# Performance work log

Hardware: AMD Instinct MI355X
Metric: run time of the kernel (lower is better)

Reference implementation:

```python
import jax, jax.numpy as jnp
import numpy as np

N = 65536          # nodes
E = 1_048_576      # edges (avg degree 16)
IN_DIM = 16        # input_irreps = 16x0e
OUT_DIM = 8        # output_irreps = 8x0e
S_MUL = 32         # hidden 0e multiplicity
V_MUL = 16         # hidden 1o multiplicity
HID = S_MUL + 3 * V_MUL  # 80
LAYERS = 3
DEG = 16.0


def fctp(feat, eattr, w1, w2, w3, w4):
    """FullyConnectedTensorProduct(hidden x '1x0e+1x1o' -> hidden) per edge.
    Paths: 0e*0e->0e, 1o*1o->0e (dot, CG 1/sqrt(3)), 0e*1o->1o, 1o*0e->1o.
    Path weights mix multiplicities; e3nn-style fan-in normalization."""
    s1 = feat[:, :S_MUL]                         # [E, 32]
    v1 = feat[:, S_MUL:].reshape(-1, V_MUL, 3)   # [E, 16, 3]
    s2 = eattr[:, 0]                             # [E]
    v2 = eattr[:, 1:4]                           # [E, 3]
    c = 1.0 / np.sqrt(2.0)  # two paths per output irrep
    out_s = c * (jnp.einsum('ea,e,ac->ec', s1, s2, w1) / np.sqrt(S_MUL)
                 + jnp.einsum('eak,ek,ac->ec', v1, v2, w2) / np.sqrt(3.0 * V_MUL))
    out_v = c * (jnp.einsum('ea,ek,ac->eck', s1, v2, w3) / np.sqrt(S_MUL)
                 + jnp.einsum('eak,e,ac->eck', v1, s2, w4) / np.sqrt(V_MUL))
    return jnp.concatenate([out_s, out_v.reshape(-1, 3 * V_MUL)], axis=-1)


def setup_inputs() -> dict:
    key = jax.random.key(0)
    ks = jax.random.split(key, 12)
    inp = {
        'x': jax.random.normal(ks[0], (N, IN_DIM), jnp.float32),
        'edge_index': jax.random.randint(ks[1], (2, E), 0, N, jnp.int64 if jax.config.jax_enable_x64 else jnp.int32),
        'edge_attr': jax.random.normal(ks[2], (E, 4), jnp.float32),
        'W_in': jax.random.normal(ks[3], (IN_DIM, HID), jnp.float32) / np.sqrt(IN_DIM),
        'b_in': jnp.zeros((HID,), jnp.float32),
        'tp_w1': jax.random.normal(ks[4], (LAYERS, S_MUL, S_MUL), jnp.float32),
        'tp_w2': jax.random.normal(ks[5], (LAYERS, V_MUL, S_MUL), jnp.float32),
        'tp_w3': jax.random.normal(ks[6], (LAYERS, S_MUL, V_MUL), jnp.float32),
        'tp_w4': jax.random.normal(ks[7], (LAYERS, V_MUL, V_MUL), jnp.float32),
        'W_out': jax.random.normal(ks[8], (HID, OUT_DIM), jnp.float32) / np.sqrt(HID),
        'b_out': jnp.zeros((OUT_DIM,), jnp.float32),
    }
    return inp


def reference(x, edge_index, edge_attr, W_in, b_in, tp_w1, tp_w2, tp_w3, tp_w4, W_out, b_out):
    src, dst = edge_index[0], edge_index[1]
    h = x @ W_in + b_in                                   # [N, 80]
    for l in range(LAYERS):
        m = fctp(h[src], edge_attr, tp_w1[l], tp_w2[l], tp_w3[l], tp_w4[l])  # [E, 80]
        h = jax.ops.segment_sum(m, dst, num_segments=N) / np.sqrt(DEG)       # [N, 80]
    h = jax.nn.relu(h)
    return h @ W_out + b_out                              # [N, 8]
```

## Files before the change

kernel.cpp:

```cpp
#include <hip/hip_runtime.h>

#define NN 65536
#define NE 1048576
#define HID 80
#define TCAP 8192
#define ECAP 8192
#define LCAP 4864

typedef unsigned int u32;
typedef unsigned short u16;
typedef unsigned long long u64;

typedef float v4f __attribute__((ext_vector_type(4)));

__device__ __forceinline__ u16 f2bf(float f) {
  u32 u = __float_as_uint(f);
  u = (u + 0x7fffu + ((u >> 16) & 1u)) >> 16;
  return (u16)u;
}
__device__ __forceinline__ float bfhi(u32 packed) {
  return __uint_as_float(packed & 0xffff0000u);
}
__device__ __forceinline__ float bflo(u32 packed) {
  return __uint_as_float(packed << 16);
}
__device__ __forceinline__ float4 ntload4f(const float4* p) {
  v4f v = __builtin_nontemporal_load((const v4f*)p);
  return make_float4(v.x, v.y, v.z, v.w);
}
__device__ __forceinline__ int ntloadi(const int* p) {
  return __builtin_nontemporal_load(p);
}

__global__ __launch_bounds__(256) void k_p1_in(const int* __restrict__ dst,
    const int* __restrict__ src, const float4* __restrict__ eattr,
    int* __restrict__ bcnt, uint4* __restrict__ tmp,
    const float* __restrict__ x, const float* __restrict__ W,
    const float* __restrict__ b, u16* __restrict__ hmain,
    u16* __restrict__ htail) {
  if (blockIdx.x < 512) {
    __shared__ int hist[256];
    __shared__ int lofs[257];
    __shared__ int gbase[256];
    __shared__ int sc[256];
    __shared__ uint4 buf[2048];
    __shared__ unsigned char bkid[2048];
    int t = threadIdx.x;
    hist[t] = 0;
    __syncthreads();
    uint4 rec[8];
    int bk[8], lr[8];
    int base = blockIdx.x * 2048 + t;
#pragma unroll
    for (int k = 0; k < 8; k++) {
      int idx = base + k * 256;
      int d = ntloadi(dst + idx);
      float4 ea = ntload4f(eattr + idx);
      int s = ntloadi(src + idx);
      u32 c01 = (u32)f2bf(ea.x) | ((u32)f2bf(ea.y) << 16);
      u32 c23 = (u32)f2bf(ea.z) | ((u32)f2bf(ea.w) << 16);
      rec[k] = make_uint4((u32)s, c01, c23, (u32)d);
      bk[k] = d >> 8;
      lr[k] = atomicAdd(&hist[bk[k]], 1);
    }
    __syncthreads();
    int h = hist[t];
    gbase[t] = atomicAdd(&bcnt[t], h);
    sc[t] = h;
    __syncthreads();
    for (int d = 1; d < 256; d <<= 1) {
      int v = (t >= d) ? sc[t - d] : 0;
      __syncthreads();
      sc[t] += v;
      __syncthreads();
    }
    lofs[t] = sc[t] - h;
    if (t == 255) lofs[256] = 2048;
    __syncthreads();
#pragma unroll
    for (int k = 0; k < 8; k++) {
      int slot = lofs[bk[k]] + lr[k];
      buf[slot] = rec[k];
      bkid[slot] = (unsigned char)bk[k];
    }
    __syncthreads();
#pragma unroll
    for (int k = 0; k < 8; k++) {
      int j = t + k * 256;
      int lo = bkid[j];
      tmp[(size_t)lo * TCAP + gbase[lo] + (j - lofs[lo])] = buf[j];
    }
  } else {
    int idx = (blockIdx.x - 512) * 256 + threadIdx.x;
    if (idx >= NN * 10) return;
    int n = idx / 10, part = idx % 10;
    const float4* xr = (const float4*)(x + (size_t)n * 16);
    float4 x0 = xr[0], x1 = xr[1], x2 = xr[2], x3 = xr[3];
    const float xs[16] = {x0.x, x0.y, x0.z, x0.w, x1.x, x1.y, x1.z, x1.w,
                          x2.x, x2.y, x2.z, x2.w, x3.x, x3.y, x3.z, x3.w};
    float acc[8];
#pragma unroll
    for (int j = 0; j < 8; j++) acc[j] = b[part * 8 + j];
#pragma unroll
    for (int k = 0; k < 16; k++) {
#pragma unroll
      for (int j = 0; j < 8; j++) acc[j] += xs[k] * W[k * HID + part * 8 + j];
    }
    u32 p0 = (u32)f2bf(acc[0]) | ((u32)f2bf(acc[1]) << 16);
    u32 p1 = (u32)f2bf(acc[2]) | ((u32)f2bf(acc[3]) << 16);
    u32 p2 = (u32)f2bf(acc[4]) | ((u32)f2bf(acc[5]) << 16);
    u32 p3 = (u32)f2bf(acc[6]) | ((u32)f2bf(acc[7]) << 16);
    uint4 vv = make_uint4(p0, p1, p2, p3);
    if (part < 8)
      *(uint4*)(hmain + (size_t)n * 64 + part * 8) = vv;
    else
      *(uint4*)(htail + (size_t)n * 16 + (part - 8) * 8) = vv;
  }
}

__global__ __launch_bounds__(512) void k_p2m(const int* __restrict__ bcnt,
    const uint4* __restrict__ tmp, int* __restrict__ counts_tot,
    int* __restrict__ offs_fin, uint4* __restrict__ erec,
    int* __restrict__ brank, int* __restrict__ bidx, int* __restrict__ dcnt) {
  extern __shared__ uint4 rbuf[];
  __shared__ int hist[256];
  __shared__ int sc[256];
  __shared__ int noff[256];
  __shared__ int cur[256];
  int t = threadIdx.x;
  if (t < 256) {
    hist[t] = 0;
    cur[t] = 0;
  }
  __syncthreads();
  int b = blockIdx.x;
  int cnt = min(bcnt[b], LCAP);
  const uint4* tb = tmp + (size_t)b * TCAP;
  for (int j = t; j < cnt; j += 512) {
    uint4 r = tb[j];
    rbuf[j] = r;
    atomicAdd(&hist[r.w & 255], 1);
  }
  __syncthreads();
  int deg = 0;
  if (t < 256) {
    deg = hist[t];
    sc[t] = (deg + 7) & ~7;
  }
  __syncthreads();
  for (int d = 1; d < 256; d <<= 1) {
    int v = (t < 256 && t >= d) ? sc[t - d] : 0;
    __syncthreads();
    if (t < 256) sc[t] += v;
    __syncthreads();
  }
  if (t < 256) {
    int p = (deg + 7) & ~7;
    int off = b * ECAP + sc[t] - p;
    noff[t] = off;
    offs_fin[b * 256 + t] = off;
    counts_tot[b * 256 + t] = deg;
  }
  __syncthreads();
  for (int j = t; j < cnt; j += 512) {
    uint4 r = rbuf[j];
    int i = r.w & 255;
    int lr = atomicAdd(&cur[i], 1);
    erec[(size_t)noff[i] + lr] = make_uint4(r.x, r.y, r.z, 0u);
  }
  __syncthreads();
  if (t < 256) {
    int degp = (deg + 7) & ~7;
    uint4 z = make_uint4(0u, 0u, 0u, 0u);
    for (int e = deg; e < degp; e++) erec[(size_t)noff[t] + e] = z;
    int n = b * 256 + t;
    int bb2 = 15 - min(degp >> 3, 15);
    int lane = t & 63;
    int base = 0;
#pragma unroll 1
    for (int bb = 0; bb < 16; bb++) {
      u64 m = __ballot(bb2 == bb);
      if (bb2 == bb) {
        int leader = __ffsll((long long)m) - 1;
        int lr = __popcll(m & ((lane == 63) ? ~0ull >> 1 : ((1ull << lane) - 1)));
        int bs = 0;
        if (lane == leader) bs = atomicAdd(&dcnt[bb], __popcll(m));
        bs = __shfl(bs, leader, 64);
        base = bs + lr;
      }
    }
    brank[n] = base;
    bidx[n] = bb2;
  }
}

__global__ __launch_bounds__(256) void k_p3(const int* __restrict__ dcnt,
    const int* __restrict__ brank, const int* __restrict__ bidx,
    int* __restrict__ nperm) {
  __shared__ int dsum[16];
  int t = threadIdx.x;
  if (t < 16) {
    int v = dcnt[t];
    int incl = v;
#pragma unroll
    for (int d = 1; d < 16; d <<= 1) {
      int o = __shfl_up(incl, d, 64);
      if (t >= d) incl += o;
    }
    dsum[t] = incl - v;
  }
  __syncthreads();
  int n = blockIdx.x * 256 + t;
  nperm[dsum[bidx[n]] + brank[n]] = n;
}

template <int LAST>
__global__ __launch_bounds__(128, 3) void k_msg(const u16* __restrict__ hmain,
    const u16* __restrict__ htail, u16* __restrict__ omain,
    u16* __restrict__ otail,
    const float* __restrict__ w1, const float* __restrict__ w2,
    const float* __restrict__ w3, const float* __restrict__ w4,
    const int* __restrict__ offsets, const int* __restrict__ counts,
    const int* __restrict__ nperm, const uint4* __restrict__ erec,
    const float* __restrict__ Wout, const float* __restrict__ bout,
    float* __restrict__ outp) {
  __shared__ float Rlds[8][4][81];
  int tid = threadIdx.x;
  const int q = tid >> 4;
  const int c = tid & 15;
  const int n = nperm[blockIdx.x * 8 + q];

  float R[4][5];
#pragma unroll
  for (int j = 0; j < 4; j++)
#pragma unroll
    for (int i = 0; i < 5; i++) R[j][i] = 0.f;

  const int start = offsets[n];
  const int degp = (counts[n] + 7) & ~7;
  const int B = degp >> 3;
  const uint2* hrow = (const uint2*)hmain + c;
  const u16* trow = htail + c;

  int i = 0;
  for (; i + 2 <= B; i += 2) {
    const int baseA = start + 8 * i;
    const int baseB = baseA + 8;
    uint4 rA[8], rB[8];
#pragma unroll
    for (int k = 0; k < 8; k++) rA[k] = erec[baseA + k];
#pragma unroll
    for (int k = 0; k < 8; k++) rB[k] = erec[baseB + k];
    uint2 hA[8], hB[8];
    u32 tA[8], tB[8];
#pragma unroll
    for (int k = 0; k < 8; k++) {
      size_t s16 = (size_t)rA[k].x * 16;
      hA[k] = hrow[s16];
      tA[k] = trow[s16];
    }
#pragma unroll
    for (int k = 0; k < 8; k++) {
      size_t s16 = (size_t)rB[k].x * 16;
      hB[k] = hrow[s16];
      tB[k] = trow[s16];
    }
#pragma unroll
    for (int k = 0; k < 8; k++) {
      float A0 = bflo(hA[k].x), A1 = bfhi(hA[k].x);
      float A2 = bflo(hA[k].y), A3 = bfhi(hA[k].y);
      float A4 = bflo(tA[k]);
      float f0 = bflo(rA[k].y), f1 = bfhi(rA[k].y);
      float f2 = bflo(rA[k].z), f3 = bfhi(rA[k].z);
      R[0][0] += f0 * A0; R[0][1] += f0 * A1; R[0][2] += f0 * A2;
      R[0][3] += f0 * A3; R[0][4] += f0 * A4;
      R[1][0] += f1 * A0; R[1][1] += f1 * A1; R[1][2] += f1 * A2;
      R[1][3] += f1 * A3; R[1][4] += f1 * A4;
      R[2][0] += f2 * A0; R[2][1] += f2 * A1; R[2][2] += f2 * A2;
      R[2][3] += f2 * A3; R[2][4] += f2 * A4;
      R[3][0] += f3 * A0; R[3][1] += f3 * A1; R[3][2] += f3 * A2;
      R[3][3] += f3 * A3; R[3][4] += f3 * A4;
    }
#pragma unroll
    for (int k = 0; k < 8; k++) {
      float A0 = bflo(hB[k].x), A1 = bfhi(hB[k].x);
      float A2 = bflo(hB[k].y), A3 = bfhi(hB[k].y);
      float A4 = bflo(tB[k]);
      float f0 = bflo(rB[k].y), f1 = bfhi(rB[k].y);
      float f2 = bflo(rB[k].z), f3 = bfhi(rB[k].z);
      R[0][0] += f0 * A0; R[0][1] += f0 * A1; R[0][2] += f0 * A2;
      R[0][3] += f0 * A3; R[0][4] += f0 * A4;
      R[1][0] += f1 * A0; R[1][1] += f1 * A1; R[1][2] += f1 * A2;
      R[1][3] += f1 * A3; R[1][4] += f1 * A4;
      R[2][0] += f2 * A0; R[2][1] += f2 * A1; R[2][2] += f2 * A2;
      R[2][3] += f2 * A3; R[2][4] += f2 * A4;
      R[3][0] += f3 * A0; R[3][1] += f3 * A1; R[3][2] += f3 * A2;
      R[3][3] += f3 * A3; R[3][4] += f3 * A4;
    }
  }
  if (i < B) {
    const int baseA = start + 8 * i;
    uint4 rA[8];
#pragma unroll
    for (int k = 0; k < 8; k++) rA[k] = erec[baseA + k];
    uint2 hA[8];
    u32 tA[8];
#pragma unroll
    for (int k = 0; k < 8; k++) {
      size_t s16 = (size_t)rA[k].x * 16;
      hA[k] = hrow[s16];
      tA[k] = trow[s16];
    }
#pragma unroll
    for (int k = 0; k < 8; k++) {
      float A0 = bflo(hA[k].x), A1 = bfhi(hA[k].x);
      float A2 = bflo(hA[k].y), A3 = bfhi(hA[k].y);
      float A4 = bflo(tA[k]);
      float f0 = bflo(rA[k].y), f1 = bfhi(rA[k].y);
      float f2 = bflo(rA[k].z), f3 = bfhi(rA[k].z);
      R[0][0] += f0 * A0; R[0][1] += f0 * A1; R[0][2] += f0 * A2;
      R[0][3] += f0 * A3; R[0][4] += f0 * A4;
      R[1][0] += f1 * A0; R[1][1] += f1 * A1; R[1][2] += f1 * A2;
      R[1][3] += f1 * A3; R[1][4] += f1 * A4;
      R[2][0] += f2 * A0; R[2][1] += f2 * A1; R[2][2] += f2 * A2;
      R[2][3] += f2 * A3; R[2][4] += f2 * A4;
      R[3][0] += f3 * A0; R[3][1] += f3 * A1; R[3][2] += f3 * A2;
      R[3][3] += f3 * A3; R[3][4] += f3 * A4;
    }
  }

#pragma unroll
  for (int j = 0; j < 4; j++) {
#pragma unroll
    for (int k = 0; k < 4; k++) Rlds[q][j][4 * c + k] = R[j][k];
    Rlds[q][j][64 + c] = R[j][4];
  }

  const float C1 = 0.03125f;
  const float C2 = 0.025515518f;
  const float C3 = 0.03125f;
  const float C4 = 0.044194174f;

  u16* opm = omain + (size_t)n * 64;

  float s0 = 0.f, s1 = 0.f;
#pragma unroll
  for (int a = 0; a < 32; a++) {
    float rs = Rlds[q][0][a];
    s0 += rs * w1[a * 32 + c];
    s1 += rs * w1[a * 32 + c + 16];
  }
  float t0 = 0.f, t1 = 0.f;
#pragma unroll
  for (int a = 0; a < 16; a++) {
    float T = Rlds[q][1][32 + 3 * a] + Rlds[q][2][33 + 3 * a] +
              Rlds[q][3][34 + 3 * a];
    t0 += T * w2[a * 32 + c];
    t1 += T * w2[a * 32 + c + 16];
  }

  float y[8];
  if (LAST) {
#pragma unroll
    for (int j = 0; j < 8; j++) y[j] = 0.f;
    float vs0 = C1 * s0 + C2 * t0;
    float vs1 = C1 * s1 + C2 * t1;
    vs0 = vs0 > 0.f ? vs0 : 0.f;
    vs1 = vs1 > 0.f ? vs1 : 0.f;
#pragma unroll
    for (int j = 0; j < 8; j++)
      y[j] += vs0 * Wout[c * 8 + j] + vs1 * Wout[(c + 16) * 8 + j];
  } else {
    opm[c] = f2bf(C1 * s0 + C2 * t0);
    opm[c + 16] = f2bf(C1 * s1 + C2 * t1);
  }

#pragma unroll
  for (int v2 = 0; v2 < 3; v2++) {
    int c2 = 32 + 16 * v2 + c;
    int cv = (c2 - 32) / 3, k = (c2 - 32) % 3;
    float a3 = 0.f, a4 = 0.f;
#pragma unroll
    for (int a = 0; a < 32; a++) a3 += Rlds[q][k + 1][a] * w3[a * 16 + cv];
#pragma unroll
    for (int a = 0; a < 16; a++)
      a4 += Rlds[q][0][32 + 3 * a + k] * w4[a * 16 + cv];
    float val = C3 * a3 + C4 * a4;
    if (LAST) {
      val = val > 0.f ? val : 0.f;
#pragma unroll
      for (int j = 0; j < 8; j++) y[j] += val * Wout[c2 * 8 + j];
    } else {
      u16 v = f2bf(val);
      if (v2 < 2) opm[32 + 16 * v2 + c] = v;
      else otail[(size_t)n * 16 + c] = v;
    }
  }

  if (LAST) {
#pragma unroll
    for (int m = 1; m <= 8; m <<= 1) {
#pragma unroll
      for (int j = 0; j < 8; j++) y[j] += __shfl_xor(y[j], m, 64);
    }
    float w = y[0];
#pragma unroll
    for (int j = 1; j < 8; j++)
      if (c == j) w = y[j];
    if (c < 8) outp[(size_t)n * 8 + c] = w + bout[c];
  }
}

extern "C" void kernel_launch(void* const* d_in, const int* in_sizes, int n_in,
                              void* d_out, int out_size, void* d_ws,
                              size_t ws_size, hipStream_t stream) {
  const float* x = (const float*)d_in[0];
  const int* ei = (const int*)d_in[1];
  const float* eattr = (const float*)d_in[2];
  const float* W_in = (const float*)d_in[3];
  const float* b_in = (const float*)d_in[4];
  const float* tp_w1 = (const float*)d_in[5];
  const float* tp_w2 = (const float*)d_in[6];
  const float* tp_w3 = (const float*)d_in[7];
  const float* tp_w4 = (const float*)d_in[8];
  const float* W_out = (const float*)d_in[9];
  const float* b_out = (const float*)d_in[10];
  float* out = (float*)d_out;

  char* ws = (char*)d_ws;
  size_t off = 0;
  auto alloc = [&](size_t bytes) {
    void* p = ws + off;
    off += (bytes + 255) & ~size_t(255);
    return p;
  };
  u16* hm_a = (u16*)alloc((size_t)NN * 64 * 2);
  u16* ht_a = (u16*)alloc((size_t)NN * 16 * 2);
  u16* hm_b = (u16*)alloc((size_t)NN * 64 * 2);
  u16* ht_b = (u16*)alloc((size_t)NN * 16 * 2);
  int* bcnt = (int*)alloc(256 * 4);
  int* dcnt = (int*)alloc(16 * 4);
  int* counts_tot = (int*)alloc((size_t)NN * 4);
  int* offs_fin = (int*)alloc((size_t)NN * 4);
  int* brank = (int*)alloc((size_t)NN * 4);
  int* bidx = (int*)alloc((size_t)NN * 4);
  int* nperm = (int*)alloc((size_t)NN * 4);
  uint4* tmp = (uint4*)alloc((size_t)256 * TCAP * 16);
  uint4* erec = (uint4*)alloc((size_t)256 * ECAP * 16);

  const int* src = ei;
  const int* dst = ei + NE;

  hipMemsetAsync(bcnt, 0, 1024 + 64, stream);
  k_p1_in<<<512 + (NN * 10 + 255) / 256, 256, 0, stream>>>(
      dst, src, (const float4*)eattr, bcnt, tmp, x, W_in, b_in, hm_a, ht_a);
  k_p2m<<<256, 512, LCAP * 16, stream>>>(bcnt, tmp, counts_tot, offs_fin,
                                         erec, brank, bidx, dcnt);
  k_p3<<<256, 256, 0, stream>>>(dcnt, brank, bidx, nperm);

  u16* hmi = hm_a;
  u16* hti = ht_a;
  u16* hmo = hm_b;
  u16* hto = ht_b;
  for (int l = 0; l < 2; l++) {
    k_msg<0><<<NN / 8, 128, 0, stream>>>(hmi, hti, hmo, hto, tp_w1 + l * 1024,
                                         tp_w2 + l * 512, tp_w3 + l * 512,
                                         tp_w4 + l * 256, offs_fin, counts_tot,
                                         nperm, erec, W_out, b_out, out);
    u16* t;
    t = hmi; hmi = hmo; hmo = t;
    t = hti; hti = hto; hto = t;
  }
  k_msg<1><<<NN / 8, 128, 0, stream>>>(hmi, hti, hmo, hto, tp_w1 + 2048,
                                       tp_w2 + 1024, tp_w3 + 1024, tp_w4 + 512,
                                       offs_fin, counts_tot, nperm, erec,
                                       W_out, b_out, out);
}
```

Baseline: 340.2 us.

## Fold input projection into first message layer by aggregating raw x

Drops the separate input-projection pass that wrote bf16 h. The first layer now gathers the 16-wide fp32 x rows directly, accumulates edge-weighted sums of x plus sums of edge attributes, and then applies W_in and b_in after aggregation. Because the input projection is linear, this gives the same result while gathering fewer bytes per edge and skipping one write and read of h. In exchange it reads fp32 x instead of bf16 h and adds a small per-node matmul in the first layer.

Result: no change. 336.8 us (-1.0%).

```diff
diff --git a/kernel.cpp b/kernel.cpp
--- a/kernel.cpp
+++ b/kernel.cpp
@@ -32,89 +32,59 @@
   return __builtin_nontemporal_load(p);
 }
 
-__global__ __launch_bounds__(256) void k_p1_in(const int* __restrict__ dst,
+__global__ __launch_bounds__(256) void k_p1(const int* __restrict__ dst,
     const int* __restrict__ src, const float4* __restrict__ eattr,
-    int* __restrict__ bcnt, uint4* __restrict__ tmp,
-    const float* __restrict__ x, const float* __restrict__ W,
-    const float* __restrict__ b, u16* __restrict__ hmain,
-    u16* __restrict__ htail) {
-  if (blockIdx.x < 512) {
-    __shared__ int hist[256];
-    __shared__ int lofs[257];
-    __shared__ int gbase[256];
-    __shared__ int sc[256];
-    __shared__ uint4 buf[2048];
-    __shared__ unsigned char bkid[2048];
-    int t = threadIdx.x;
-    hist[t] = 0;
+    int* __restrict__ bcnt, uint4* __restrict__ tmp) {
+  __shared__ int hist[256];
+  __shared__ int lofs[257];
+  __shared__ int gbase[256];
+  __shared__ int sc[256];
+  __shared__ uint4 buf[2048];
+  __shared__ unsigned char bkid[2048];
+  int t = threadIdx.x;
+  hist[t] = 0;
+  __syncthreads();
+  uint4 rec[8];
+  int bk[8], lr[8];
+  int base = blockIdx.x * 2048 + t;
+#pragma unroll
+  for (int k = 0; k < 8; k++) {
+    int idx = base + k * 256;
+    int d = ntloadi(dst + idx);
+    float4 ea = ntload4f(eattr + idx);
+    int s = ntloadi(src + idx);
+    u32 c01 = (u32)f2bf(ea.x) | ((u32)f2bf(ea.y) << 16);
+    u32 c23 = (u32)f2bf(ea.z) | ((u32)f2bf(ea.w) << 16);
+    rec[k] = make_uint4((u32)s, c01, c23, (u32)d);
+    bk[k] = d >> 8;
+    lr[k] = atomicAdd(&hist[bk[k]], 1);
+  }
+  __syncthreads();
+  int h = hist[t];
+  gbase[t] = atomicAdd(&bcnt[t], h);
+  sc[t] = h;
+  __syncthreads();
+  for (int d = 1; d < 256; d <<= 1) {
+    int v = (t >= d) ? sc[t - d] : 0;
     __syncthreads();
-    uint4 rec[8];
-    int bk[8], lr[8];
-    int base = blockIdx.x * 2048 + t;
-#pragma unroll
-    for (int k = 0; k < 8; k++) {
-      int idx = base + k * 256;
-      int d = ntloadi(dst + idx);
-      float4 ea = ntload4f(eattr + idx);
-      int s = ntloadi(src + idx);
-      u32 c01 = (u32)f2bf(ea.x) | ((u32)f2bf(ea.y) << 16);
-      u32 c23 = (u32)f2bf(ea.z) | ((u32)f2bf(ea.w) << 16);
-      rec[k] = make_uint4((u32)s, c01, c23, (u32)d);
-      bk[k] = d >> 8;
-      lr[k] = atomicAdd(&hist[bk[k]], 1);
-    }
+    sc[t] += v;
     __syncthreads();
-    int h = hist[t];
-    gbase[t] = atomicAdd(&bcnt[t], h);
-    sc[t] = h;
-    __syncthreads();
-    for (int d = 1; d < 256; d <<= 1) {
-      int v = (t >= d) ? sc[t - d] : 0;
-      __syncthreads();
-      sc[t] += v;
-      __syncthreads();
-    }
-    lofs[t] = sc[t] - h;
-    if (t == 255) lofs[256] = 2048;
-    __syncthreads();
-#pragma unroll
-    for (int k = 0; k < 8; k++) {
-      int slot = lofs[bk[k]] + lr[k];
-      buf[slot] = rec[k];
-      bkid[slot] = (unsigned char)bk[k];
-    }
-    __syncthreads();
-#pragma unroll
-    for (int k = 0; k < 8; k++) {
-      int j = t + k * 256;
-      int lo = bkid[j];
-      tmp[(size_t)lo * TCAP + gbase[lo] + (j - lofs[lo])] = buf[j];
-    }
-  } else {
-    int idx = (blockIdx.x - 512) * 256 + threadIdx.x;
-    if (idx >= NN * 10) return;
-    int n = idx / 10, part = idx % 10;
-    const float4* xr = (const float4*)(x + (size_t)n * 16);
-    float4 x0 = xr[0], x1 = xr[1], x2 = xr[2], x3 = xr[3];
-    const float xs[16] = {x0.x, x0.y, x0.z, x0.w, x1.x, x1.y, x1.z, x1.w,
-                          x2.x, x2.y, x2.z, x2.w, x3.x, x3.y, x3.z, x3.w};
-    float acc[8];
-#pragma unroll
-    for (int j = 0; j < 8; j++) acc[j] = b[part * 8 + j];
-#pragma unroll
-    for (int k = 0; k < 16; k++) {
-#pragma unroll
-      for (int j = 0; j < 8; j++) acc[j] += xs[k] * W[k * HID + part * 8 + j];
-    }
-    u32 p0 = (u32)f2bf(acc[0]) | ((u32)f2bf(acc[1]) << 16);
-    u32 p1 = (u32)f2bf(acc[2]) | ((u32)f2bf(acc[3]) << 16);
-    u32 p2 = (u32)f2bf(acc[4]) | ((u32)f2bf(acc[5]) << 16);
-    u32 p3 = (u32)f2bf(acc[6]) | ((u32)f2bf(acc[7]) << 16);
-    uint4 vv = make_uint4(p0, p1, p2, p3);
-    if (part < 8)
-      *(uint4*)(hmain + (size_t)n * 64 + part * 8) = vv;
-    else
-      *(uint4*)(htail + (size_t)n * 16 + (part - 8) * 8) = vv;
+  }
+  lofs[t] = sc[t] - h;
+  if (t == 255) lofs[256] = 2048;
+  __syncthreads();
+#pragma unroll
+  for (int k = 0; k < 8; k++) {
+    int slot = lofs[bk[k]] + lr[k];
+    buf[slot] = rec[k];
+    bkid[slot] = (unsigned char)bk[k];
+  }
+  __syncthreads();
+#pragma unroll
+  for (int k = 0; k < 8; k++) {
+    int j = t + k * 256;
+    int lo = bkid[j];
+    tmp[(size_t)lo * TCAP + gbase[lo] + (j - lofs[lo])] = buf[j];
   }
 }
 
@@ -214,7 +184,7 @@
   nperm[dsum[bidx[n]] + brank[n]] = n;
 }
 
-template <int LAST>
+template <int LAST, int FIRST>
 __global__ __launch_bounds__(128, 3) void k_msg(const u16* __restrict__ hmain,
     const u16* __restrict__ htail, u16* __restrict__ omain,
     u16* __restrict__ otail,
@@ -223,117 +193,201 @@
     const int* __restrict__ offsets, const int* __restrict__ counts,
     const int* __restrict__ nperm, const uint4* __restrict__ erec,
     const float* __restrict__ Wout, const float* __restrict__ bout,
-    float* __restrict__ outp) {
+    float* __restrict__ outp,
+    const float* __restrict__ xg, const float* __restrict__ Win,
+    const float* __restrict__ bin) {
   __shared__ float Rlds[8][4][81];
+  __shared__ float Mlds[8][4][16];
   int tid = threadIdx.x;
   const int q = tid >> 4;
   const int c = tid & 15;
   const int n = nperm[blockIdx.x * 8 + q];
 
-  float R[4][5];
-#pragma unroll
-  for (int j = 0; j < 4; j++)
-#pragma unroll
-    for (int i = 0; i < 5; i++) R[j][i] = 0.f;
-
   const int start = offsets[n];
   const int degp = (counts[n] + 7) & ~7;
   const int B = degp >> 3;
-  const uint2* hrow = (const uint2*)hmain + c;
-  const u16* trow = htail + c;
-
-  int i = 0;
-  for (; i + 2 <= B; i += 2) {
-    const int baseA = start + 8 * i;
-    const int baseB = baseA + 8;
-    uint4 rA[8], rB[8];
-#pragma unroll
-    for (int k = 0; k < 8; k++) rA[k] = erec[baseA + k];
-#pragma unroll
-    for (int k = 0; k < 8; k++) rB[k] = erec[baseB + k];
-    uint2 hA[8], hB[8];
-    u32 tA[8], tB[8];
-#pragma unroll
-    for (int k = 0; k < 8; k++) {
-      size_t s16 = (size_t)rA[k].x * 16;
-      hA[k] = hrow[s16];
-      tA[k] = trow[s16];
-    }
-#pragma unroll
-    for (int k = 0; k < 8; k++) {
-      size_t s16 = (size_t)rB[k].x * 16;
-      hB[k] = hrow[s16];
-      tB[k] = trow[s16];
-    }
-#pragma unroll
-    for (int k = 0; k < 8; k++) {
-      float A0 = bflo(hA[k].x), A1 = bfhi(hA[k].x);
-      float A2 = bflo(hA[k].y), A3 = bfhi(hA[k].y);
-      float A4 = bflo(tA[k]);
-      float f0 = bflo(rA[k].y), f1 = bfhi(rA[k].y);
-      float f2 = bflo(rA[k].z), f3 = bfhi(rA[k].z);
-      R[0][0] += f0 * A0; R[0][1] += f0 * A1; R[0][2] += f0 * A2;
-      R[0][3] += f0 * A3; R[0][4] += f0 * A4;
-      R[1][0] += f1 * A0; R[1][1] += f1 * A1; R[1][2] += f1 * A2;
-      R[1][3] += f1 * A3; R[1][4] += f1 * A4;
-      R[2][0] += f2 * A0; R[2][1] += f2 * A1; R[2][2] += f2 * A2;
-      R[2][3] += f2 * A3; R[2][4] += f2 * A4;
-      R[3][0] += f3 * A0; R[3][1] += f3 * A1; R[3][2] += f3 * A2;
-      R[3][3] += f3 * A3; R[3][4] += f3 * A4;
-    }
-#pragma unroll
-    for (int k = 0; k < 8; k++) {
-      float A0 = bflo(hB[k].x), A1 = bfhi(hB[k].x);
-      float A2 = bflo(hB[k].y), A3 = bfhi(hB[k].y);
-      float A4 = bflo(tB[k]);
-      float f0 = bflo(rB[k].y), f1 = bfhi(rB[k].y);
-      float f2 = bflo(rB[k].z), f3 = bfhi(rB[k].z);
-      R[0][0] += f0 * A0; R[0][1] += f0 * A1; R[0][2] += f0 * A2;
-      R[0][3] += f0 * A3; R[0][4] += f0 * A4;
-      R[1][0] += f1 * A0; R[1][1] += f1 * A1; R[1][2] += f1 * A2;
-      R[1][3] += f1 * A3; R[1][4] += f1 * A4;
-      R[2][0] += f2 * A0; R[2][1] += f2 * A1; R[2][2] += f2 * A2;
-      R[2][3] += f2 * A3; R[2][4] += f2 * A4;
-      R[3][0] += f3 * A0; R[3][1] += f3 * A1; R[3][2] += f3 * A2;
-      R[3][3] += f3 * A3; R[3][4] += f3 * A4;
-    }
-  }
-  if (i < B) {
-    const int baseA = start + 8 * i;
-    uint4 rA[8];
-#pragma unroll
-    for (int k = 0; k < 8; k++) rA[k] = erec[baseA + k];
-    uint2 hA[8];
-    u32 tA[8];
-#pragma unroll
-    for (int k = 0; k < 8; k++) {
-      size_t s16 = (size_t)rA[k].x * 16;
-      hA[k] = hrow[s16];
-      tA[k] = trow[s16];
-    }
-#pragma unroll
-    for (int k = 0; k < 8; k++) {
-      float A0 = bflo(hA[k].x), A1 = bfhi(hA[k].x);
-      float A2 = bflo(hA[k].y), A3 = bfhi(hA[k].y);
-      float A4 = bflo(tA[k]);
-      float f0 = bflo(rA[k].y), f1 = bfhi(rA[k].y);
-      float f2 = bflo(rA[k].z), f3 = bfhi(rA[k].z);
-      R[0][0] += f0 * A0; R[0][1] += f0 * A1; R[0][2] += f0 * A2;
-      R[0][3] += f0 * A3; R[0][4] += f0 * A4;
-      R[1][0] += f1 * A0; R[1][1] += f1 * A1; R[1][2] += f1 * A2;
-      R[1][3] += f1 * A3; R[1][4] += f1 * A4;
-      R[2][0] += f2 * A0; R[2][1] += f2 * A1; R[2][2] += f2 * A2;
-      R[2][3] += f2 * A3; R[2][4] += f2 * A4;
-      R[3][0] += f3 * A0; R[3][1] += f3 * A1; R[3][2] += f3 * A2;
-      R[3][3] += f3 * A3; R[3][4] += f3 * A4;
-    }
-  }
-
-#pragma unroll
-  for (int j = 0; j < 4; j++) {
-#pragma unroll
-    for (int k = 0; k < 4; k++) Rlds[q][j][4 * c + k] = R[j][k];
-    Rlds[q][j][64 + c] = R[j][4];
+
+  if (FIRST) {
+    float M0 = 0.f, M1 = 0.f, M2 = 0.f, M3 = 0.f;
+    float a0 = 0.f, a1 = 0.f, a2 = 0.f, a3 = 0.f;
+    const float* xrow = xg + c;
+    int i = 0;
+    for (; i + 2 <= B; i += 2) {
+      const int baseA = start + 8 * i;
+      const int baseB = baseA + 8;
+      uint4 rA[8], rB[8];
+#pragma unroll
+      for (int k = 0; k < 8; k++) rA[k] = erec[baseA + k];
+#pragma unroll
+      for (int k = 0; k < 8; k++) rB[k] = erec[baseB + k];
+      float xA[8], xB[8];
+#pragma unroll
+      for (int k = 0; k < 8; k++) xA[k] = xrow[(size_t)rA[k].x * 16];
+#pragma unroll
+      for (int k = 0; k < 8; k++) xB[k] = xrow[(size_t)rB[k].x * 16];
+#pragma unroll
+      for (int k = 0; k < 8; k++) {
+        float f0 = bflo(rA[k].y), f1 = bfhi(rA[k].y);
+        float f2 = bflo(rA[k].z), f3 = bfhi(rA[k].z);
+        M0 += f0 * xA[k]; M1 += f1 * xA[k];
+        M2 += f2 * xA[k]; M3 += f3 * xA[k];
+        a0 += f0; a1 += f1; a2 += f2; a3 += f3;
+      }
+#pragma unroll
+      for (int k = 0; k < 8; k++) {
+        float f0 = bflo(rB[k].y), f1 = bfhi(rB[k].y);
+        float f2 = bflo(rB[k].z), f3 = bfhi(rB[k].z);
+        M0 += f0 * xB[k]; M1 += f1 * xB[k];
+        M2 += f2 * xB[k]; M3 += f3 * xB[k];
+        a0 += f0; a1 += f1; a2 += f2; a3 += f3;
+      }
+    }
+    if (i < B) {
+      const int baseA = start + 8 * i;
+      uint4 rA[8];
+#pragma unroll
+      for (int k = 0; k < 8; k++) rA[k] = erec[baseA + k];
+      float xA[8];
+#pragma unroll
+      for (int k = 0; k < 8; k++) xA[k] = xrow[(size_t)rA[k].x * 16];
+#pragma unroll
+      for (int k = 0; k < 8; k++) {
+        float f0 = bflo(rA[k].y), f1 = bfhi(rA[k].y);
+        float f2 = bflo(rA[k].z), f3 = bfhi(rA[k].z);
+        M0 += f0 * xA[k]; M1 += f1 * xA[k];
+        M2 += f2 * xA[k]; M3 += f3 * xA[k];
+        a0 += f0; a1 += f1; a2 += f2; a3 += f3;
+      }
+    }
+    Mlds[q][0][c] = M0;
+    Mlds[q][1][c] = M1;
+    Mlds[q][2][c] = M2;
+    Mlds[q][3][c] = M3;
+#pragma unroll
+    for (int s2 = 0; s2 < 5; s2++) {
+      int a = (s2 < 4) ? (4 * c + s2) : (64 + c);
+      float bb = bin[a];
+      float r0 = a0 * bb, r1 = a1 * bb, r2 = a2 * bb, r3 = a3 * bb;
+#pragma unroll
+      for (int cc = 0; cc < 16; cc++) {
+        float w = Win[cc * HID + a];
+        r0 += Mlds[q][0][cc] * w;
+        r1 += Mlds[q][1][cc] * w;
+        r2 += Mlds[q][2][cc] * w;
+        r3 += Mlds[q][3][cc] * w;
+      }
+      if (s2 < 4) {
+        Rlds[q][0][4 * c + s2] = r0;
+        Rlds[q][1][4 * c + s2] = r1;
+        Rlds[q][2][4 * c + s2] = r2;
+        Rlds[q][3][4 * c + s2] = r3;
+      } else {
+        Rlds[q][0][64 + c] = r0;
+        Rlds[q][1][64 + c] = r1;
+        Rlds[q][2][64 + c] = r2;
+        Rlds[q][3][64 + c] = r3;
+      }
+    }
+  } else {
+    float R[4][5];
+#pragma unroll
+    for (int j = 0; j < 4; j++)
+#pragma unroll
+      for (int i2 = 0; i2 < 5; i2++) R[j][i2] = 0.f;
+    const uint2* hrow = (const uint2*)hmain + c;
+    const u16* trow = htail + c;
+    int i = 0;
+    for (; i + 2 <= B; i += 2) {
+      const int baseA = start + 8 * i;
+      const int baseB = baseA + 8;
+      uint4 rA[8], rB[8];
+#pragma unroll
+      for (int k = 0; k < 8; k++) rA[k] = erec[baseA + k];
+#pragma unroll
+      for (int k = 0; k < 8; k++) rB[k] = erec[baseB + k];
+      uint2 hA[8], hB[8];
+      u32 tA[8], tB[8];
+#pragma unroll
+      for (int k = 0; k < 8; k++) {
+        size_t s16 = (size_t)rA[k].x * 16;
+        hA[k] = hrow[s16];
+        tA[k] = trow[s16];
+      }
+#pragma unroll
+      for (int k = 0; k < 8; k++) {
+        size_t s16 = (size_t)rB[k].x * 16;
+        hB[k] = hrow[s16];
+        tB[k] = trow[s16];
+      }
+#pragma unroll
+      for (int k = 0; k < 8; k++) {
+        float A0 = bflo(hA[k].x), A1 = bfhi(hA[k].x);
+        float A2 = bflo(hA[k].y), A3 = bfhi(hA[k].y);
+        float A4 = bflo(tA[k]);
+        float f0 = bflo(rA[k].y), f1 = bfhi(rA[k].y);
+        float f2 = bflo(rA[k].z), f3 = bfhi(rA[k].z);
+        R[0][0] += f0 * A0; R[0][1] += f0 * A1; R[0][2] += f0 * A2;
+        R[0][3] += f0 * A3; R[0][4] += f0 * A4;
+        R[1][0] += f1 * A0; R[1][1] += f1 * A1; R[1][2] += f1 * A2;
+        R[1][3] += f1 * A3; R[1][4] += f1 * A4;
+        R[2][0] += f2 * A0; R[2][1] += f2 * A1; R[2][2] += f2 * A2;
+        R[2][3] += f2 * A3; R[2][4] += f2 * A4;
+        R[3][0] += f3 * A0; R[3][1] += f3 * A1; R[3][2] += f3 * A2;
+        R[3][3] += f3 * A3; R[3][4] += f3 * A4;
+      }
+#pragma unroll
+      for (int k = 0; k < 8; k++) {
+        float A0 = bflo(hB[k].x), A1 = bfhi(hB[k].x);
+        float A2 = bflo(hB[k].y), A3 = bfhi(hB[k].y);
+        float A4 = bflo(tB[k]);
+        float f0 = bflo(rB[k].y), f1 = bfhi(rB[k].y);
+        float f2 = bflo(rB[k].z), f3 = bfhi(rB[k].z);
+        R[0][0] += f0 * A0; R[0][1] += f0 * A1; R[0][2] += f0 * A2;
+        R[0][3] += f0 * A3; R[0][4] += f0 * A4;
+        R[1][0] += f1 * A0; R[1][1] += f1 * A1; R[1][2] += f1 * A2;
+        R[1][3] += f1 * A3; R[1][4] += f1 * A4;
+        R[2][0] += f2 * A0; R[2][1] += f2 * A1; R[2][2] += f2 * A2;
+        R[2][3] += f2 * A3; R[2][4] += f2 * A4;
+        R[3][0] += f3 * A0; R[3][1] += f3 * A1; R[3][2] += f3 * A2;
+        R[3][3] += f3 * A3; R[3][4] += f3 * A4;
+      }
+    }
+    if (i < B) {
+      const int baseA = start + 8 * i;
+      uint4 rA[8];
+#pragma unroll
+      for (int k = 0; k < 8; k++) rA[k] = erec[baseA + k];
+      uint2 hA[8];
+      u32 tA[8];
+#pragma unroll
+      for (int k = 0; k < 8; k++) {
+        size_t s16 = (size_t)rA[k].x * 16;
+        hA[k] = hrow[s16];
+        tA[k] = trow[s16];
+      }
+#pragma unroll
+      for (int k = 0; k < 8; k++) {
+        float A0 = bflo(hA[k].x), A1 = bfhi(hA[k].x);
+        float A2 = bflo(hA[k].y), A3 = bfhi(hA[k].y);
+        float A4 = bflo(tA[k]);
+        float f0 = bflo(rA[k].y), f1 = bfhi(rA[k].y);
+        float f2 = bflo(rA[k].z), f3 = bfhi(rA[k].z);
+        R[0][0] += f0 * A0; R[0][1] += f0 * A1; R[0][2] += f0 * A2;
+        R[0][3] += f0 * A3; R[0][4] += f0 * A4;
+        R[1][0] += f1 * A0; R[1][1] += f1 * A1; R[1][2] += f1 * A2;
+        R[1][3] += f1 * A3; R[1][4] += f1 * A4;
+        R[2][0] += f2 * A0; R[2][1] += f2 * A1; R[2][2] += f2 * A2;
+        R[2][3] += f2 * A3; R[2][4] += f2 * A4;
+        R[3][0] += f3 * A0; R[3][1] += f3 * A1; R[3][2] += f3 * A2;
+        R[3][3] += f3 * A3; R[3][4] += f3 * A4;
+      }
+    }
+#pragma unroll
+    for (int j = 0; j < 4; j++) {
+#pragma unroll
+      for (int k = 0; k < 4; k++) Rlds[q][j][4 * c + k] = R[j][k];
+      Rlds[q][j][64 + c] = R[j][4];
+    }
   }
 
   const float C1 = 0.03125f;
@@ -452,27 +506,20 @@
   const int* dst = ei + NE;
 
   hipMemsetAsync(bcnt, 0, 1024 + 64, stream);
-  k_p1_in<<<512 + (NN * 10 + 255) / 256, 256, 0, stream>>>(
-      dst, src, (const float4*)eattr, bcnt, tmp, x, W_in, b_in, hm_a, ht_a);
+  k_p1<<<512, 256, 0, stream>>>(dst, src, (const float4*)eattr, bcnt, tmp);
   k_p2m<<<256, 512, LCAP * 16, stream>>>(bcnt, tmp, counts_tot, offs_fin,
                                          erec, brank, bidx, dcnt);
   k_p3<<<256, 256, 0, stream>>>(dcnt, brank, bidx, nperm);
 
-  u16* hmi = hm_a;
-  u16* hti = ht_a;
-  u16* hmo = hm_b;
-  u16* hto = ht_b;
-  for (int l = 0; l < 2; l++) {
-    k_msg<0><<<NN / 8, 128, 0, stream>>>(hmi, hti, hmo, hto, tp_w1 + l * 1024,
-                                         tp_w2 + l * 512, tp_w3 + l * 512,
-                                         tp_w4 + l * 256, offs_fin, counts_tot,
-                                         nperm, erec, W_out, b_out, out);
-    u16* t;
-    t = hmi; hmi = hmo; hmo = t;
-    t = hti; hti = hto; hto = t;
-  }
-  k_msg<1><<<NN / 8, 128, 0, stream>>>(hmi, hti, hmo, hto, tp_w1 + 2048,
-                                       tp_w2 + 1024, tp_w3 + 1024, tp_w4 + 512,
-                                       offs_fin, counts_tot, nperm, erec,
-                                       W_out, b_out, out);
-}
+  k_msg<0, 1><<<NN / 8, 128, 0, stream>>>(
+      nullptr, nullptr, hm_b, ht_b, tp_w1, tp_w2, tp_w3, tp_w4, offs_fin,
+      counts_tot, nperm, erec, W_out, b_out, out, x, W_in, b_in);
+  k_msg<0, 0><<<NN / 8, 128, 0, stream>>>(
+      hm_b, ht_b, hm_a, ht_a, tp_w1 + 1024, tp_w2 + 512, tp_w3 + 512,
+      tp_w4 + 256, offs_fin, counts_tot, nperm, erec, W_out, b_out, out, x,
+      W_in, b_in);
+  k_msg<1, 0><<<NN / 8, 128, 0, stream>>>(
+      hm_a, ht_a, hm_b, ht_b, tp_w1 + 2048, tp_w2 + 1024, tp_w3 + 1024,
+      tp_w4 + 512, offs_fin, counts_tot, nperm, erec, W_out, b_out, out, x,
+      W_in, b_in);
+}
```
